# Optimization experiments

Measured on AMD Instinct MI355X. Metric: run time of the kernel, lower is better.

The kernel has to match this reference:

```python
import jax, jax.numpy as jnp
import numpy as np

B, S, E, H = 8, 2048, 512, 8
D = E // H  # head_dim = 64


def setup_inputs() -> dict:
    key0 = jax.random.key(0)
    ks = jax.random.split(key0, 12)
    scale = 1.0 / np.sqrt(E)
    return {
        "value": jax.random.normal(ks[0], (B, S, E), jnp.float32),
        "key": jax.random.normal(ks[1], (B, S, E), jnp.float32),
        "query": jax.random.normal(ks[2], (B, S, E), jnp.float32),
        "mask": jax.random.randint(ks[3], (B, 1, 1, S), 0, 2, jnp.int32),
        "wq": jax.random.normal(ks[4], (E, E), jnp.float32) * scale,
        "bq": jnp.zeros((E,), jnp.float32),
        "wk": jax.random.normal(ks[5], (E, E), jnp.float32) * scale,
        "bk": jnp.zeros((E,), jnp.float32),
        "wv": jax.random.normal(ks[6], (E, E), jnp.float32) * scale,
        "bv": jnp.zeros((E,), jnp.float32),
        "wo": jax.random.normal(ks[7], (E, E), jnp.float32) * scale,
        "bo": jnp.zeros((E,), jnp.float32),
    }


def reference(value, key, query, mask, wq, bq, wk, bk, wv, bv, wo, bo):
    b, s, e = query.shape
    # projections
    q = (query @ wq + bq).reshape(b, s, H, D)  # (B,S,H,D)
    k = (key @ wk + bk).reshape(b, s, H, D)
    v = (value @ wv + bv).reshape(b, s, H, D)
    # scaled dot-product logits: (B,H,Sq,Sk)
    logits = jnp.einsum("bqhd,bkhd->bhqk", q, k) / jnp.sqrt(jnp.asarray(D, q.dtype))
    logits = logits + mask.astype(logits.dtype) * -1e9  # mask==1 -> blocked
    attn = jax.nn.softmax(logits, axis=-1)
    out = jnp.einsum("bhqk,bkhd->bqhd", attn, v).reshape(b, s, e)
    return out @ wo + bo
```

## Files before the change

### kernel.cpp

```cpp
#include <hip/hip_runtime.h>

#define Bz 8
#define Sz 2048
#define Ez 512
#define Hz 8
#define Dz 64

typedef _Float16 f16;
typedef __attribute__((ext_vector_type(2))) _Float16 f16x2;
typedef __attribute__((ext_vector_type(8))) _Float16 f16x8;
typedef __attribute__((ext_vector_type(4))) float f32x4;

#define LOG2E 1.44269504f

__device__ __forceinline__ void async16(const void* g, void* l) {
    __builtin_amdgcn_global_load_lds(
        (const __attribute__((address_space(1))) unsigned int*)g,
        (__attribute__((address_space(3))) unsigned int*)l, 16, 0, 0);
}

__device__ __forceinline__ f16x2 pkrtz(float a, float b) {
    return __builtin_bit_cast(f16x2, __builtin_amdgcn_cvt_pkrtz(a, b));
}

__device__ __forceinline__ int swz(int row) {
    return (row & 7) ^ ((2 * ((row >> 3) & 3)) & 7);
}

__global__ __launch_bounds__(256)
void cast_kernel(const float* __restrict__ q, const float* __restrict__ k,
                 const float* __restrict__ v,
                 f16* __restrict__ qa, f16* __restrict__ ka, f16* __restrict__ va)
{
    const int z = blockIdx.y;
    const int idx = blockIdx.x * 256 + threadIdx.x;
    const float* src = (z == 0) ? q : (z == 1) ? k : v;
    f16* dst = (z == 0) ? qa : (z == 1) ? ka : va;
    float4 x = *(const float4*)&src[(size_t)idx * 4];
    f16x2 h0 = pkrtz(x.x, x.y), h1 = pkrtz(x.z, x.w);
    f16 h[4] = {h0[0], h0[1], h1[0], h1[1]};
    *(uint2*)&dst[(size_t)idx * 4] = *(uint2*)h;
}

__global__ __launch_bounds__(256)
void prep_w(const float* __restrict__ W0, const float* __restrict__ W1,
            const float* __restrict__ W2, const float* __restrict__ W3,
            f16* __restrict__ T0, f16* __restrict__ T1,
            f16* __restrict__ T2, f16* __restrict__ T3)
{
    __shared__ float S[64][68];
    const float* W = (blockIdx.z==0)?W0:(blockIdx.z==1)?W1:(blockIdx.z==2)?W2:W3;
    f16*         T = (blockIdx.z==0)?T0:(blockIdx.z==1)?T1:(blockIdx.z==2)?T2:T3;
    const float sc = (blockIdx.z == 0) ? 0.125f * LOG2E : 1.0f;
    const int k0 = blockIdx.x * 64, n0 = blockIdx.y * 64;
    const int tid = threadIdx.x;
    {
        int kr = tid >> 4, nc = (tid & 15) * 4;
        #pragma unroll
        for (int i = 0; i < 4; ++i) {
            float4 w4 = *(const float4*)&W[(size_t)(k0 + kr + i*16) * Ez + n0 + nc];
            S[kr + i*16][nc+0] = w4.x; S[kr + i*16][nc+1] = w4.y;
            S[kr + i*16][nc+2] = w4.z; S[kr + i*16][nc+3] = w4.w;
        }
    }
    __syncthreads();
    {
        int n = tid >> 2, kq = tid & 3;
        f16 h[16];
        #pragma unroll
        for (int j = 0; j < 16; ++j) h[j] = (f16)(S[kq*16 + j][n] * sc);
        f16* dst = &T[(size_t)(n0 + n) * Ez + k0 + kq*16];
        *(uint4*)&dst[0] = *(uint4*)&h[0];
        *(uint4*)&dst[8] = *(uint4*)&h[8];
    }
}

__global__ __launch_bounds__(256)
void mask_index(const int* __restrict__ mask, int* __restrict__ idx,
                int* __restrict__ slen)
{
    __shared__ int sc2[2][256];
    __shared__ int stot;
    const int b = blockIdx.x, tid = threadIdx.x;
    const int* mp = mask + (size_t)b * Sz;
    int m[8], c = 0;
    #pragma unroll
    for (int j = 0; j < 8; ++j) { m[j] = mp[tid*8 + j]; c += (m[j] == 0); }
    sc2[0][tid] = c;
    __syncthreads();
    int src = 0;
    #pragma unroll
    for (int s = 1; s < 256; s <<= 1) {
        int v = sc2[src][tid] + ((tid >= s) ? sc2[src][tid - s] : 0);
        sc2[src ^ 1][tid] = v;
        src ^= 1;
        __syncthreads();
    }
    int incl = sc2[src][tid];
    int base = incl - c;
    if (tid == 255) { slen[b] = incl; stot = incl; }
    int k = base;
    #pragma unroll
    for (int j = 0; j < 8; ++j)
        if (m[j] == 0) idx[(size_t)b * Sz + (k++)] = tid*8 + j;
    __syncthreads();
    for (int j = stot + tid; j < Sz; j += 256) idx[(size_t)b * Sz + j] = 0;
}

__global__ __launch_bounds__(256)
void compact_v(const f16* __restrict__ vp, const int* __restrict__ idx,
               const int* __restrict__ slen, f16* __restrict__ vt)
{
    const int ct = blockIdx.x, h = blockIdx.y, b = blockIdx.z;
    const int sl = slen[b];
    if (ct * 64 >= sl) {
        if (ct > 0 || sl > 0) return;
    }
    __shared__ f16 S[64 * 72];
    const int tid = threadIdx.x;
    {
        int r = tid >> 2, ch = tid & 3;
        int j = ct * 64 + r;
        uint4 v0 = {0,0,0,0}, v1 = {0,0,0,0};
        if (j < sl) {
            int s = idx[(size_t)b * Sz + j];
            const f16* srcp = vp + (((size_t)b * Hz + h) * Sz + s) * Dz + ch * 16;
            v0 = *(const uint4*)&srcp[0];
            v1 = *(const uint4*)&srcp[8];
        }
        *(uint4*)&S[r*72 + ch*16]     = v0;
        *(uint4*)&S[r*72 + ch*16 + 8] = v1;
    }
    __syncthreads();
    {
        int d = tid >> 2, kq = tid & 3;
        f16 hh[16];
        #pragma unroll
        for (int j = 0; j < 16; ++j) hh[j] = S[(kq*16 + j)*72 + d];
        f16* dst = vt + (((size_t)b * Hz + h) * Dz + d) * Sz + ct*64 + kq*16;
        *(uint4*)&dst[0] = *(uint4*)&hh[0];
        *(uint4*)&dst[8] = *(uint4*)&hh[8];
    }
}

__global__ __launch_bounds__(256, 4)
void proj_gemm(const f16* __restrict__ qa, const f16* __restrict__ ka,
               const f16* __restrict__ va,
               const f16* __restrict__ wtq, const f16* __restrict__ wtk,
               const f16* __restrict__ wtv,
               const float* __restrict__ bqp, const float* __restrict__ bkp,
               const float* __restrict__ bvp,
               f16* __restrict__ qp, f16* __restrict__ kp, f16* __restrict__ vp)
{
    __shared__ __align__(16) char lds[18432];
    const int z = blockIdx.z;
    const f16* A  = (z==0)?qa:(z==1)?ka:va;
    const f16* Wt = (z==0)?wtq:(z==1)?wtk:wtv;
    const float* bias = (z==0)?bqp:(z==1)?bkp:bvp;
    f16* C16 = (z==0)?qp:(z==1)?kp:vp;
    const float bscale = (z==0) ? 0.125f*LOG2E : 1.0f;

    const int tid  = threadIdx.x;
    const int lane = tid & 63, w = tid >> 6;
    const int col  = lane & 15, quad = lane >> 4;
    const int wm = w & 1, wn = w >> 1;
    const int m0 = blockIdx.x * 128, n0 = blockIdx.y * 128;
    const int srow = lane >> 2, schunk = lane & 3;

    f16* As = (f16*)lds;
    f16* Ws = As + 4096;

    f32x4 acc[4][4];
    #pragma unroll
    for (int i = 0; i < 4; ++i)
        #pragma unroll
        for (int j = 0; j < 4; ++j) acc[i][j] = (f32x4){0.f,0.f,0.f,0.f};

    const int xrc = (col >> 1) & 3;

    for (int t = 0; t < 16; ++t) {
        __syncthreads();
        #pragma unroll
        for (int i = 0; i < 2; ++i) {
            int row = w*32 + i*16 + srow;
            int cl = schunk ^ ((row >> 1) & 3);
            async16(&A[(size_t)(m0 + row) * Ez + t*32 + cl*8],  &As[row*32 + schunk*8]);
            async16(&Wt[(size_t)(n0 + row) * Ez + t*32 + cl*8], &Ws[row*32 + schunk*8]);
        }
        __syncthreads();
        f16x8 af[4];
        #pragma unroll
        for (int mi = 0; mi < 4; ++mi)
            af[mi] = *(const f16x8*)&As[(wm*64 + mi*16 + col)*32 + ((quad ^ xrc)*8)];
        #pragma unroll
        for (int ni = 0; ni < 4; ++ni) {
            f16x8 wf = *(const f16x8*)&Ws[(wn*64 + ni*16 + col)*32 + ((quad ^ xrc)*8)];
            #pragma unroll
            for (int mi = 0; mi < 4; ++mi)
                acc[mi][ni] = __builtin_amdgcn_mfma_f32_16x16x32_f16(af[mi], wf, acc[mi][ni], 0,0,0);
        }
    }

    f16* Tr = (f16*)lds;
    #pragma unroll
    for (int p = 0; p < 2; ++p) {
        __syncthreads();
        if (wn == p) {
            #pragma unroll
            for (int ni = 0; ni < 4; ++ni) {
                float bv = bias[n0 + p*64 + ni*16 + col] * bscale;
                #pragma unroll
                for (int mi = 0; mi < 4; ++mi)
                    #pragma unroll
                    for (int rr = 0; rr < 4; ++rr) {
                        int ml = wm*64 + mi*16 + quad*4 + rr;
                        Tr[ml*72 + ni*16 + col] = (f16)(acc[mi][ni][rr] + bv);
                    }
            }
        }
        __syncthreads();
        int rw = tid >> 1, half = tid & 1;
        int m = m0 + rw, b = m >> 11, s = m & (Sz-1);
        int hh = (n0 >> 6) + p;
        f16* dst = &C16[(((size_t)b*Hz + hh)*Sz + s)*Dz + half*32];
        const f16* srcp = &Tr[rw*72 + half*32];
        #pragma unroll
        for (int j = 0; j < 4; ++j)
            *(uint4*)&dst[j*8] = *(const uint4*)&srcp[j*8];
    }
}

__global__ __launch_bounds__(256, 4)
void out_gemm(const f16* __restrict__ A, const f16* __restrict__ Wt,
              const float* __restrict__ bias, float* __restrict__ Cf)
{
    __shared__ __align__(16) char lds[16384];
    const int tid  = threadIdx.x;
    const int lane = tid & 63, w = tid >> 6;
    const int col  = lane & 15, quad = lane >> 4;
    const int wm = w & 1, wn = w >> 1;
    const int m0 = blockIdx.x * 128, n0 = blockIdx.y * 128;
    const int srow = lane >> 2, schunk = lane & 3;

    f16* As = (f16*)lds;
    f16* Ws = As + 4096;

    f32x4 acc[4][4];
    #pragma unroll
    for (int i = 0; i < 4; ++i)
        #pragma unroll
        for (int j = 0; j < 4; ++j) acc[i][j] = (f32x4){0.f,0.f,0.f,0.f};

    const int xrc = (col >> 1) & 3;

    for (int t = 0; t < 16; ++t) {
        __syncthreads();
        #pragma unroll
        for (int i = 0; i < 2; ++i) {
            int row = w*32 + i*16 + srow;
            int cl = schunk ^ ((row >> 1) & 3);
            async16(&A[(size_t)(m0 + row) * Ez + t*32 + cl*8],  &As[row*32 + schunk*8]);
            async16(&Wt[(size_t)(n0 + row) * Ez + t*32 + cl*8], &Ws[row*32 + schunk*8]);
        }
        __syncthreads();
        f16x8 af[4];
        #pragma unroll
        for (int mi = 0; mi < 4; ++mi)
            af[mi] = *(const f16x8*)&As[(wm*64 + mi*16 + col)*32 + ((quad ^ xrc)*8)];
        #pragma unroll
        for (int ni = 0; ni < 4; ++ni) {
            f16x8 wf = *(const f16x8*)&Ws[(wn*64 + ni*16 + col)*32 + ((quad ^ xrc)*8)];
            #pragma unroll
            for (int mi = 0; mi < 4; ++mi)
                acc[mi][ni] = __builtin_amdgcn_mfma_f32_16x16x32_f16(af[mi], wf, acc[mi][ni], 0,0,0);
        }
    }

    #pragma unroll
    for (int ni = 0; ni < 4; ++ni) {
        int n = n0 + wn*64 + ni*16 + col;
        float bv = bias[n];
        #pragma unroll
        for (int mi = 0; mi < 4; ++mi)
            #pragma unroll
            for (int rr = 0; rr < 4; ++rr) {
                int m = m0 + wm*64 + mi*16 + quad*4 + rr;
                Cf[(size_t)m * Ez + n] = acc[mi][ni][rr] + bv;
            }
    }
}

__global__ __launch_bounds__(256, 4)
void attn_f16(const f16* __restrict__ Q, const f16* __restrict__ K,
              const f16* __restrict__ VT, const int* __restrict__ idx,
              const int* __restrict__ slen, f16* __restrict__ O)
{
    __shared__ __align__(16) f16 KS[2][64*64];
    __shared__ __align__(16) f16 VS[2][64*64];

    const int tid  = threadIdx.x;
    const int lane = tid & 63, w = tid >> 6;
    const int col  = lane & 15, quad = lane >> 4;

    const int blk = blockIdx.x;
    const int xcd = blk & 7, slot = blk >> 3;
    const int bh = xcd + 8 * (slot >> 4);
    const int qb = slot & 15;
    const int b = bh >> 3, h = bh & 7;

    const int sl = slen[b];
    const int nt = (sl + 63) >> 6;

    const int q0 = qb * 128 + w * 32;

    f16x8 qf[2][2];
    #pragma unroll
    for (int qt = 0; qt < 2; ++qt)
        #pragma unroll
        for (int ks = 0; ks < 2; ++ks)
            qf[qt][ks] = *(const f16x8*)&Q[((size_t)bh*Sz + q0 + qt*16 + col)*Dz + ks*32 + quad*8];

    const f16* Kp = K + (size_t)bh * Sz * Dz;
    const f16* Vp = VT + (size_t)bh * Dz * Sz;
    const int* ixp = idx + (size_t)b * Sz;

    const int srow = lane >> 3, sch = lane & 7;
    const int row0 = w*16 + srow, row1 = row0 + 8;
    const int g0 = swz(row0), g1 = swz(row1);
    const int cl0 = sch ^ g0, cl1 = sch ^ g1;

    int keyrow[4], gk[4];
    #pragma unroll
    for (int kc = 0; kc < 4; ++kc) {
        keyrow[kc] = 32*(kc>>1) + 8*(col>>2) + 4*(kc&1) + (col&3);
        gk[kc] = swz(keyrow[kc]);
    }

    f32x4 oacc[2][4];
    #pragma unroll
    for (int qt = 0; qt < 2; ++qt)
        #pragma unroll
        for (int dc = 0; dc < 4; ++dc) oacc[qt][dc] = (f32x4){0.f,0.f,0.f,0.f};
    float lsum[2] = {0.f, 0.f};

    auto issue = [&](int t, int buf, int s0, int s1) {
        async16(&Kp[(size_t)s0*Dz + cl0*8],          &KS[buf][row0*64 + sch*8]);
        async16(&Vp[(size_t)row0*Sz + t*64 + cl0*8], &VS[buf][row0*64 + sch*8]);
        async16(&Kp[(size_t)s1*Dz + cl1*8],          &KS[buf][row1*64 + sch*8]);
        async16(&Vp[(size_t)row1*Sz + t*64 + cl1*8], &VS[buf][row1*64 + sch*8]);
    };

    int cs0 = ixp[row0], cs1 = ixp[row1];
    issue(0, 0, cs0, cs1);
    int ns0 = 0, ns1 = 0;
    if (nt > 1) { ns0 = ixp[64 + row0]; ns1 = ixp[64 + row1]; }

    for (int t = 0; t < nt; ++t) {
        const int cur = t & 1;
        __syncthreads();
        if (t + 1 < nt) {
            issue(t + 1, cur ^ 1, ns0, ns1);
            if (t + 2 < nt) {
                ns0 = ixp[(t+2)*64 + row0];
                ns1 = ixp[(t+2)*64 + row1];
            }
        }

        f32x4 sc[2][4];
        #pragma unroll
        for (int qt = 0; qt < 2; ++qt)
            #pragma unroll
            for (int kc = 0; kc < 4; ++kc) sc[qt][kc] = (f32x4){0.f,0.f,0.f,0.f};
        #pragma unroll
        for (int kc = 0; kc < 4; ++kc) {
            #pragma unroll
            for (int ks = 0; ks < 2; ++ks) {
                f16x8 kf = *(const f16x8*)&KS[cur][keyrow[kc]*64 + (((ks*4 + quad) ^ gk[kc])*8)];
                sc[0][kc] = __builtin_amdgcn_mfma_f32_16x16x32_f16(kf, qf[0][ks], sc[0][kc], 0,0,0);
                sc[1][kc] = __builtin_amdgcn_mfma_f32_16x16x32_f16(kf, qf[1][ks], sc[1][kc], 0,0,0);
            }
        }

        const bool last = (t == nt - 1);
        union { f16x2 h2[4]; f16x8 h8; } ph[2][2];
        #pragma unroll
        for (int qt = 0; qt < 2; ++qt) {
            #pragma unroll
            for (int kg = 0; kg < 2; ++kg) {
                float e0 = exp2f(sc[qt][2*kg][0]), e1 = exp2f(sc[qt][2*kg][1]);
                float e2 = exp2f(sc[qt][2*kg][2]), e3 = exp2f(sc[qt][2*kg][3]);
                float e4 = exp2f(sc[qt][2*kg+1][0]), e5 = exp2f(sc[qt][2*kg+1][1]);
                float e6 = exp2f(sc[qt][2*kg+1][2]), e7 = exp2f(sc[qt][2*kg+1][3]);
                float ls;
                if (last) {
                    int rem = sl - t*64 - 32*kg - 8*quad;
                    ls = ((rem > 0 ? e0 : 0.f) + (rem > 1 ? e1 : 0.f))
                       + ((rem > 2 ? e2 : 0.f) + (rem > 3 ? e3 : 0.f))
                       + ((rem > 4 ? e4 : 0.f) + (rem > 5 ? e5 : 0.f))
                       + ((rem > 6 ? e6 : 0.f) + (rem > 7 ? e7 : 0.f));
                } else {
                    ls = ((e0 + e1) + (e2 + e3)) + ((e4 + e5) + (e6 + e7));
                }
                lsum[qt] += ls;
                ph[qt][kg].h2[0] = pkrtz(e0, e1);
                ph[qt][kg].h2[1] = pkrtz(e2, e3);
                ph[qt][kg].h2[2] = pkrtz(e4, e5);
                ph[qt][kg].h2[3] = pkrtz(e6, e7);
            }
        }

        #pragma unroll
        for (int dc = 0; dc < 4; ++dc) {
            const int d = dc*16 + col;
            const int gd = swz(d);
            #pragma unroll
            for (int kg = 0; kg < 2; ++kg) {
                f16x8 vf = *(const f16x8*)&VS[cur][d*64 + (((kg*4 + quad) ^ gd)*8)];
                oacc[0][dc] = __builtin_amdgcn_mfma_f32_16x16x32_f16(vf, ph[0][kg].h8, oacc[0][dc], 0,0,0);
                oacc[1][dc] = __builtin_amdgcn_mfma_f32_16x16x32_f16(vf, ph[1][kg].h8, oacc[1][dc], 0,0,0);
            }
        }
    }

    float inv[2];
    #pragma unroll
    for (int qt = 0; qt < 2; ++qt) {
        float v = lsum[qt];
        v += __shfl_xor(v, 16, 64);
        v += __shfl_xor(v, 32, 64);
        inv[qt] = 1.0f / v;
    }
    #pragma unroll
    for (int qt = 0; qt < 2; ++qt) {
        const int q = q0 + qt*16 + col;
        f16* op = &O[((size_t)b*Sz + q)*Ez + h*Dz];
        #pragma unroll
        for (int dc = 0; dc < 4; ++dc) {
            f16 ov[4] = {(f16)(oacc[qt][dc][0]*inv[qt]), (f16)(oacc[qt][dc][1]*inv[qt]),
                         (f16)(oacc[qt][dc][2]*inv[qt]), (f16)(oacc[qt][dc][3]*inv[qt])};
            *(uint2*)&op[dc*16 + quad*4] = *(uint2*)ov;
        }
    }
}

extern "C" void kernel_launch(void* const* d_in, const int* in_sizes, int n_in,
                              void* d_out, int out_size, void* d_ws, size_t ws_size,
                              hipStream_t stream)
{
    const float* value = (const float*)d_in[0];
    const float* key   = (const float*)d_in[1];
    const float* query = (const float*)d_in[2];
    const int*   mask  = (const int*)d_in[3];
    const float* wq = (const float*)d_in[4];
    const float* bq = (const float*)d_in[5];
    const float* wk = (const float*)d_in[6];
    const float* bk = (const float*)d_in[7];
    const float* wv = (const float*)d_in[8];
    const float* bv = (const float*)d_in[9];
    const float* wo = (const float*)d_in[10];
    const float* bo = (const float*)d_in[11];
    float* out = (float*)d_out;

    const size_t nW   = (size_t)Ez * Ez;
    const size_t nAct = (size_t)Bz * Sz * Ez;
    f16* wtq = (f16*)d_ws;
    f16* wtk = wtq + nW;
    f16* wtv = wtk + nW;
    f16* wto = wtv + nW;
    f16* qa  = wto + nW;
    f16* ka  = qa + nAct;
    f16* va  = ka + nAct;
    f16* qp  = va + nAct;
    f16* kp  = qp + nAct;
    f16* vp  = kp + nAct;
    f16* vt  = vp + nAct;
    f16* o16 = vt + nAct;
    int* idxp = (int*)(o16 + nAct);
    int* slenp = idxp + Bz * Sz;

    cast_kernel<<<dim3(8192, 3), 256, 0, stream>>>(query, key, value, qa, ka, va);
    prep_w<<<dim3(8, 8, 4), 256, 0, stream>>>(wq, wk, wv, wo, wtq, wtk, wtv, wto);
    mask_index<<<Bz, 256, 0, stream>>>(mask, idxp, slenp);

    proj_gemm<<<dim3(128, 4, 3), 256, 0, stream>>>(qa, ka, va, wtq, wtk, wtv,
                                                   bq, bk, bv, qp, kp, vp);

    compact_v<<<dim3(32, Hz, Bz), 256, 0, stream>>>(vp, idxp, slenp, vt);

    attn_f16<<<1024, 256, 0, stream>>>(qp, kp, vt, idxp, slenp, o16);

    out_gemm<<<dim3(128, 4), 256, 0, stream>>>(o16, wto, bo, out);
}
```

Baseline: 300.5 us.

## Double-buffer GEMM tiles, fold mask indexing into cast kernel, tidy attention

Both projection and output GEMMs now use double-buffered LDS tiles. The next K-slice is issued asynchronously before computing the current one, which removes one barrier per iteration and overlaps loads with MFMA work. The mask prefix-scan kernel is merged into the cast kernel as an extra grid slice to save a launch, though it adds 8188 early-exit blocks. The attention score MFMA is restructured to start from a zero accumulator, and nt is clamped to at least 1. Doubling LDS to 32KB per GEMM block may reduce occupancy.

```diff
diff --git a/kernel.cpp b/kernel.cpp
--- a/kernel.cpp
+++ b/kernel.cpp
@@ -29,17 +29,49 @@
 
 __global__ __launch_bounds__(256)
 void cast_kernel(const float* __restrict__ q, const float* __restrict__ k,
-                 const float* __restrict__ v,
-                 f16* __restrict__ qa, f16* __restrict__ ka, f16* __restrict__ va)
+                 const float* __restrict__ v, const int* __restrict__ mask,
+                 f16* __restrict__ qa, f16* __restrict__ ka, f16* __restrict__ va,
+                 int* __restrict__ idx, int* __restrict__ slen)
 {
     const int z = blockIdx.y;
-    const int idx = blockIdx.x * 256 + threadIdx.x;
+    const int tid = threadIdx.x;
+    if (z == 3) {
+        const int b = blockIdx.x;
+        if (b >= Bz) return;
+        __shared__ int sc2[2][256];
+        __shared__ int stot;
+        const int* mp = mask + (size_t)b * Sz;
+        int m[8], c = 0;
+        #pragma unroll
+        for (int j = 0; j < 8; ++j) { m[j] = mp[tid*8 + j]; c += (m[j] == 0); }
+        sc2[0][tid] = c;
+        __syncthreads();
+        int src = 0;
+        #pragma unroll
+        for (int s = 1; s < 256; s <<= 1) {
+            int vv = sc2[src][tid] + ((tid >= s) ? sc2[src][tid - s] : 0);
+            sc2[src ^ 1][tid] = vv;
+            src ^= 1;
+            __syncthreads();
+        }
+        int incl = sc2[src][tid];
+        int base = incl - c;
+        if (tid == 255) { slen[b] = incl; stot = incl; }
+        int kk = base;
+        #pragma unroll
+        for (int j = 0; j < 8; ++j)
+            if (m[j] == 0) idx[(size_t)b * Sz + (kk++)] = tid*8 + j;
+        __syncthreads();
+        for (int j = stot + tid; j < Sz; j += 256) idx[(size_t)b * Sz + j] = 0;
+        return;
+    }
+    const int i = blockIdx.x * 256 + tid;
     const float* src = (z == 0) ? q : (z == 1) ? k : v;
     f16* dst = (z == 0) ? qa : (z == 1) ? ka : va;
-    float4 x = *(const float4*)&src[(size_t)idx * 4];
+    float4 x = *(const float4*)&src[(size_t)i * 4];
     f16x2 h0 = pkrtz(x.x, x.y), h1 = pkrtz(x.z, x.w);
     f16 h[4] = {h0[0], h0[1], h1[0], h1[1]};
-    *(uint2*)&dst[(size_t)idx * 4] = *(uint2*)h;
+    *(uint2*)&dst[(size_t)i * 4] = *(uint2*)h;
 }
 
 __global__ __launch_bounds__(256)
@@ -76,46 +108,12 @@
 }
 
 __global__ __launch_bounds__(256)
-void mask_index(const int* __restrict__ mask, int* __restrict__ idx,
-                int* __restrict__ slen)
-{
-    __shared__ int sc2[2][256];
-    __shared__ int stot;
-    const int b = blockIdx.x, tid = threadIdx.x;
-    const int* mp = mask + (size_t)b * Sz;
-    int m[8], c = 0;
-    #pragma unroll
-    for (int j = 0; j < 8; ++j) { m[j] = mp[tid*8 + j]; c += (m[j] == 0); }
-    sc2[0][tid] = c;
-    __syncthreads();
-    int src = 0;
-    #pragma unroll
-    for (int s = 1; s < 256; s <<= 1) {
-        int v = sc2[src][tid] + ((tid >= s) ? sc2[src][tid - s] : 0);
-        sc2[src ^ 1][tid] = v;
-        src ^= 1;
-        __syncthreads();
-    }
-    int incl = sc2[src][tid];
-    int base = incl - c;
-    if (tid == 255) { slen[b] = incl; stot = incl; }
-    int k = base;
-    #pragma unroll
-    for (int j = 0; j < 8; ++j)
-        if (m[j] == 0) idx[(size_t)b * Sz + (k++)] = tid*8 + j;
-    __syncthreads();
-    for (int j = stot + tid; j < Sz; j += 256) idx[(size_t)b * Sz + j] = 0;
-}
-
-__global__ __launch_bounds__(256)
 void compact_v(const f16* __restrict__ vp, const int* __restrict__ idx,
                const int* __restrict__ slen, f16* __restrict__ vt)
 {
     const int ct = blockIdx.x, h = blockIdx.y, b = blockIdx.z;
     const int sl = slen[b];
-    if (ct * 64 >= sl) {
-        if (ct > 0 || sl > 0) return;
-    }
+    if (ct * 64 >= sl && !(ct == 0 && sl == 0)) return;
     __shared__ f16 S[64 * 72];
     const int tid = threadIdx.x;
     {
@@ -152,7 +150,7 @@
                const float* __restrict__ bvp,
                f16* __restrict__ qp, f16* __restrict__ kp, f16* __restrict__ vp)
 {
-    __shared__ __align__(16) char lds[18432];
+    __shared__ __align__(16) char lds[32768];
     const int z = blockIdx.z;
     const f16* A  = (z==0)?qa:(z==1)?ka:va;
     const f16* Wt = (z==0)?wtq:(z==1)?wtk:wtv;
@@ -167,19 +165,15 @@
     const int m0 = blockIdx.x * 128, n0 = blockIdx.y * 128;
     const int srow = lane >> 2, schunk = lane & 3;
 
-    f16* As = (f16*)lds;
-    f16* Ws = As + 4096;
-
     f32x4 acc[4][4];
     #pragma unroll
     for (int i = 0; i < 4; ++i)
         #pragma unroll
         for (int j = 0; j < 4; ++j) acc[i][j] = (f32x4){0.f,0.f,0.f,0.f};
 
-    const int xrc = (col >> 1) & 3;
-
-    for (int t = 0; t < 16; ++t) {
-        __syncthreads();
+    auto issue = [&](int t, int buf) {
+        f16* As = (f16*)(lds + buf * 16384);
+        f16* Ws = As + 4096;
         #pragma unroll
         for (int i = 0; i < 2; ++i) {
             int row = w*32 + i*16 + srow;
@@ -187,7 +181,17 @@
             async16(&A[(size_t)(m0 + row) * Ez + t*32 + cl*8],  &As[row*32 + schunk*8]);
             async16(&Wt[(size_t)(n0 + row) * Ez + t*32 + cl*8], &Ws[row*32 + schunk*8]);
         }
-        __syncthreads();
+    };
+
+    issue(0, 0);
+    const int xrc = (col >> 1) & 3;
+
+    for (int t = 0; t < 16; ++t) {
+        const int cur = t & 1;
+        __syncthreads();
+        if (t < 15) issue(t + 1, cur ^ 1);
+        f16* As = (f16*)(lds + cur * 16384);
+        f16* Ws = As + 4096;
         f16x8 af[4];
         #pragma unroll
         for (int mi = 0; mi < 4; ++mi)
@@ -234,7 +238,7 @@
 void out_gemm(const f16* __restrict__ A, const f16* __restrict__ Wt,
               const float* __restrict__ bias, float* __restrict__ Cf)
 {
-    __shared__ __align__(16) char lds[16384];
+    __shared__ __align__(16) char lds[32768];
     const int tid  = threadIdx.x;
     const int lane = tid & 63, w = tid >> 6;
     const int col  = lane & 15, quad = lane >> 4;
@@ -242,19 +246,15 @@
     const int m0 = blockIdx.x * 128, n0 = blockIdx.y * 128;
     const int srow = lane >> 2, schunk = lane & 3;
 
-    f16* As = (f16*)lds;
-    f16* Ws = As + 4096;
-
     f32x4 acc[4][4];
     #pragma unroll
     for (int i = 0; i < 4; ++i)
         #pragma unroll
         for (int j = 0; j < 4; ++j) acc[i][j] = (f32x4){0.f,0.f,0.f,0.f};
 
-    const int xrc = (col >> 1) & 3;
-
-    for (int t = 0; t < 16; ++t) {
-        __syncthreads();
+    auto issue = [&](int t, int buf) {
+        f16* As = (f16*)(lds + buf * 16384);
+        f16* Ws = As + 4096;
         #pragma unroll
         for (int i = 0; i < 2; ++i) {
             int row = w*32 + i*16 + srow;
@@ -262,7 +262,17 @@
             async16(&A[(size_t)(m0 + row) * Ez + t*32 + cl*8],  &As[row*32 + schunk*8]);
             async16(&Wt[(size_t)(n0 + row) * Ez + t*32 + cl*8], &Ws[row*32 + schunk*8]);
         }
-        __syncthreads();
+    };
+
+    issue(0, 0);
+    const int xrc = (col >> 1) & 3;
+
+    for (int t = 0; t < 16; ++t) {
+        const int cur = t & 1;
+        __syncthreads();
+        if (t < 15) issue(t + 1, cur ^ 1);
+        f16* As = (f16*)(lds + cur * 16384);
+        f16* Ws = As + 4096;
         f16x8 af[4];
         #pragma unroll
         for (int mi = 0; mi < 4; ++mi)
@@ -309,7 +319,8 @@
     const int b = bh >> 3, h = bh & 7;
 
     const int sl = slen[b];
-    const int nt = (sl + 63) >> 6;
+    int nt = (sl + 63) >> 6;
+    if (nt < 1) nt = 1;
 
     const int q0 = qb * 128 + w * 32;
 
@@ -326,8 +337,7 @@
 
     const int srow = lane >> 3, sch = lane & 7;
     const int row0 = w*16 + srow, row1 = row0 + 8;
-    const int g0 = swz(row0), g1 = swz(row1);
-    const int cl0 = sch ^ g0, cl1 = sch ^ g1;
+    const int cl0 = sch ^ swz(row0), cl1 = sch ^ swz(row1);
 
     int keyrow[4], gk[4];
     #pragma unroll
@@ -342,6 +352,7 @@
         #pragma unroll
         for (int dc = 0; dc < 4; ++dc) oacc[qt][dc] = (f32x4){0.f,0.f,0.f,0.f};
     float lsum[2] = {0.f, 0.f};
+    const f32x4 zero4 = (f32x4){0.f, 0.f, 0.f, 0.f};
 
     auto issue = [&](int t, int buf, int s0, int s1) {
         async16(&Kp[(size_t)s0*Dz + cl0*8],          &KS[buf][row0*64 + sch*8]);
@@ -368,17 +379,13 @@
 
         f32x4 sc[2][4];
         #pragma unroll
-        for (int qt = 0; qt < 2; ++qt)
-            #pragma unroll
-            for (int kc = 0; kc < 4; ++kc) sc[qt][kc] = (f32x4){0.f,0.f,0.f,0.f};
-        #pragma unroll
         for (int kc = 0; kc < 4; ++kc) {
-            #pragma unroll
-            for (int ks = 0; ks < 2; ++ks) {
-                f16x8 kf = *(const f16x8*)&KS[cur][keyrow[kc]*64 + (((ks*4 + quad) ^ gk[kc])*8)];
-                sc[0][kc] = __builtin_amdgcn_mfma_f32_16x16x32_f16(kf, qf[0][ks], sc[0][kc], 0,0,0);
-                sc[1][kc] = __builtin_amdgcn_mfma_f32_16x16x32_f16(kf, qf[1][ks], sc[1][kc], 0,0,0);
-            }
+            f16x8 kf0 = *(const f16x8*)&KS[cur][keyrow[kc]*64 + ((quad ^ gk[kc])*8)];
+            f16x8 kf1 = *(const f16x8*)&KS[cur][keyrow[kc]*64 + (((4 + quad) ^ gk[kc])*8)];
+            sc[0][kc] = __builtin_amdgcn_mfma_f32_16x16x32_f16(kf0, qf[0][0], zero4, 0,0,0);
+            sc[1][kc] = __builtin_amdgcn_mfma_f32_16x16x32_f16(kf0, qf[1][0], zero4, 0,0,0);
+            sc[0][kc] = __builtin_amdgcn_mfma_f32_16x16x32_f16(kf1, qf[0][1], sc[0][kc], 0,0,0);
+            sc[1][kc] = __builtin_amdgcn_mfma_f32_16x16x32_f16(kf1, qf[1][1], sc[1][kc], 0,0,0);
         }
 
         const bool last = (t == nt - 1);
@@ -478,9 +485,9 @@
     int* idxp = (int*)(o16 + nAct);
     int* slenp = idxp + Bz * Sz;
 
-    cast_kernel<<<dim3(8192, 3), 256, 0, stream>>>(query, key, value, qa, ka, va);
+    cast_kernel<<<dim3(8192, 4), 256, 0, stream>>>(query, key, value, mask,
+                                                   qa, ka, va, idxp, slenp);
     prep_w<<<dim3(8, 8, 4), 256, 0, stream>>>(wq, wk, wv, wo, wtq, wtk, wtv, wto);
-    mask_index<<<Bz, 256, 0, stream>>>(mask, idxp, slenp);
 
     proj_gemm<<<dim3(128, 4, 3), 256, 0, stream>>>(qa, ka, va, wtq, wtk, wtv,
                                                    bq, bk, bv, qp, kp, vp);
```

Measured after the change: 290.9 us. -3.2%, faster.
